# Kernel tuning notes

Measured on AMD Instinct MI355X. Metric: run time of the kernel, lower is better.

## Reference

```python
import jax, jax.numpy as jnp
import numpy as np

B, N, C, H, NRES = 32, 1024, 384, 1024, 20
NTAB = 21  # 20 aa + unknown, per AlphaFold residue_constants


def setup_inputs() -> dict:
    key = jax.random.key(0)
    ks = jax.random.split(key, 16)
    s = 0.02
    inp = {}
    inp['act'] = jax.random.normal(ks[0], (B, N, C), jnp.float32)
    inp['angles'] = jax.random.normal(ks[1], (B, N, 7, 2), jnp.float32)
    inp['rigids'] = jax.random.normal(ks[2], (B, N, 7), jnp.float32)
    inp['fixed_mask'] = jax.random.randint(ks[3], (B, N), 0, 2, jnp.int32)
    inp['seq_t'] = jax.random.randint(ks[4], (B, N), 0, NRES, jnp.int32)
    inp['residx_atom37_to_atom14'] = jax.random.randint(ks[5], (B, N, 37), 0, 14, jnp.int32)
    inp['ln_g'] = jnp.ones((C,), jnp.float32)
    inp['ln_b'] = jnp.zeros((C,), jnp.float32)
    inp['w1'] = jax.random.normal(ks[6], (C, H), jnp.float32) * s
    inp['b1'] = jnp.zeros((H,), jnp.float32)
    inp['w2'] = jax.random.normal(ks[7], (H, H), jnp.float32) * s
    inp['b2'] = jnp.zeros((H,), jnp.float32)
    inp['w3'] = jax.random.normal(ks[8], (H, NRES), jnp.float32) * s
    inp['b3'] = jnp.zeros((NRES,), jnp.float32)
    # stand-in residue_constants tables (same shapes/dtypes as AlphaFold's)
    inp['default_frames'] = jax.random.normal(ks[9], (NTAB, 8, 4, 4), jnp.float32)
    inp['group_idx'] = jax.random.randint(ks[10], (NTAB, 14), 0, 8, jnp.int32)
    inp['atom14_mask'] = (jax.random.uniform(ks[11], (NTAB, 14)) > 0.3).astype(jnp.float32)
    inp['atom37_mask'] = (jax.random.uniform(ks[12], (NTAB, 37)) > 0.3).astype(jnp.float32)
    inp['lit_positions'] = jax.random.normal(ks[13], (NTAB, 14, 3), jnp.float32)
    return inp


def quat_to_rot(q):
    q = q / jnp.sqrt(jnp.sum(q * q, axis=-1, keepdims=True) + 1e-8)
    w, x, y, z = q[..., 0], q[..., 1], q[..., 2], q[..., 3]
    r = jnp.stack([
        1 - 2 * (y * y + z * z), 2 * (x * y - w * z), 2 * (x * z + w * y),
        2 * (x * y + w * z), 1 - 2 * (x * x + z * z), 2 * (y * z - w * x),
        2 * (x * z - w * y), 2 * (y * z + w * x), 1 - 2 * (x * x + y * y)
    ], axis=-1)
    return r.reshape(q.shape[:-1] + (3, 3))


def compose(r1, t1, r2, t2):
    # rigid composition: (r1, t1) o (r2, t2)
    return (jnp.einsum('...ij,...jk->...ik', r1, r2),
            jnp.einsum('...ij,...j->...i', r1, t2) + t1)


def reference(act, angles, rigids, fixed_mask, seq_t, residx_atom37_to_atom14,
              ln_g, ln_b, w1, b1, w2, b2, w3, b3,
              default_frames, group_idx, atom14_mask, atom37_mask, lit_positions):
    # --- small MLP head ---
    mu = jnp.mean(act, axis=-1, keepdims=True)
    var = jnp.var(act, axis=-1, keepdims=True)
    h = (act - mu) / jnp.sqrt(var + 1e-5) * ln_g + ln_b
    h = jax.nn.relu(h @ w1 + b1)
    h = jax.nn.relu(h @ w2 + b2)
    logits = h @ w3 + b3                                # [B,N,20]
    p_0t = jax.nn.softmax(logits, axis=-1)
    seq0 = jnp.argmax(p_0t, axis=-1).astype(jnp.int32)
    seq0 = seq0 * (1 - fixed_mask) + seq_t * fixed_mask  # [B,N]

    # --- backbone frame from quaternion rigids ---
    rb = quat_to_rot(rigids[..., :4])                    # [B,N,3,3]
    tb = rigids[..., 4:]                                 # [B,N,3]

    # --- torsion_angles_to_frames ---
    df = default_frames[seq0]                            # [B,N,8,4,4]
    dr, dt = df[..., :3, :3], df[..., :3, 3]
    sin, cos = angles[..., 0], angles[..., 1]            # [B,N,7]
    z1 = jnp.zeros_like(sin[..., :1])
    sin8 = jnp.concatenate([z1, sin], axis=-1)           # backbone group has angle 0
    cos8 = jnp.concatenate([jnp.ones_like(z1), cos], axis=-1)
    zz, oo = jnp.zeros_like(sin8), jnp.ones_like(sin8)
    rx = jnp.stack([oo, zz, zz, zz, cos8, -sin8, zz, sin8, cos8], axis=-1)
    rx = rx.reshape(sin8.shape + (3, 3))                 # rotation about x-axis
    fr = jnp.einsum('bngij,bngjk->bngik', dr, rx)        # frames to backbone (pre-chain)
    ft = dt
    # chain chi2->chi1, chi3->chi2, chi4->chi3
    r5, t5 = compose(fr[..., 4, :, :], ft[..., 4, :], fr[..., 5, :, :], ft[..., 5, :])
    r6, t6 = compose(r5, t5, fr[..., 6, :, :], ft[..., 6, :])
    r7, t7 = compose(r6, t6, fr[..., 7, :, :], ft[..., 7, :])
    frot = jnp.concatenate([fr[..., :5, :, :], r5[..., None, :, :], r6[..., None, :, :], r7[..., None, :, :]], axis=-3)
    ftr = jnp.concatenate([ft[..., :5, :], t5[..., None, :], t6[..., None, :], t7[..., None, :]], axis=-2)
    grot, gtr = compose(rb[..., None, :, :], tb[..., None, :], frot, ftr)  # [B,N,8,3,3],[B,N,8,3]

    # --- frames_and_literature_positions_to_atom14_pos ---
    gi = group_idx[seq0]                                 # [B,N,14]
    ar = jnp.take_along_axis(grot, jnp.broadcast_to(gi[..., None, None], gi.shape + (3, 3)), axis=2)
    at = jnp.take_along_axis(gtr, jnp.broadcast_to(gi[..., None], gi.shape + (3,)), axis=2)
    lit = lit_positions[seq0]                            # [B,N,14,3]
    m14 = atom14_mask[seq0]                              # [B,N,14]
    pred = (jnp.einsum('bnaij,bnaj->bnai', ar, lit) + at) * m14[..., None]

    # --- atom14 -> atom37 gather ---
    idx = residx_atom37_to_atom14
    final = jnp.take_along_axis(pred, jnp.broadcast_to(idx[..., None], idx.shape + (3,)), axis=2)
    m37 = atom37_mask[seq0]                              # [B,N,37]
    return logits, seq0, pred, final, m14, m37
```

## Files before the change

kernel.cpp:

```cpp
#include <hip/hip_runtime.h>
#include <math.h>

#define B_ 32
#define N_ 1024
#define C_ 384
#define H_ 1024
#define NRES 20
#define NTAB 21
#define M_TOTAL (B_*N_)
#define BK 32

typedef __attribute__((ext_vector_type(8))) short bf16x8;
typedef __attribute__((ext_vector_type(4))) float f32x4;

#define GLOAD_LDS(gptr, lptr) \
    __builtin_amdgcn_global_load_lds( \
        (const __attribute__((address_space(1))) void*)(gptr), \
        (__attribute__((address_space(3))) void*)(lptr), 16, 0, 0)

__device__ inline short bf16_rne(float v) {
    unsigned u = __float_as_uint(v);
    unsigned r = u + 0x7fffu + ((u >> 16) & 1u);
    return (short)(r >> 16);
}
__device__ inline void split2(float v, short& h, short& l) {
    unsigned u = __float_as_uint(v);
    unsigned r = (u + 0x7fffu + ((u >> 16) & 1u)) & 0xffff0000u;
    h = (short)(r >> 16);
    l = bf16_rne(v - __uint_as_float(r));
}

__global__ __launch_bounds__(256) void ln_split_kernel(const float* __restrict__ act,
                                                       const float* __restrict__ lng,
                                                       const float* __restrict__ lnb,
                                                       short* __restrict__ Xh,
                                                       short* __restrict__ Xl) {
    int wave = threadIdx.x >> 6;
    int lane = threadIdx.x & 63;
    int row  = blockIdx.x * 4 + wave;
    const float* x = act + (size_t)row * C_;
    float v[6];
    float s = 0.f;
#pragma unroll
    for (int i = 0; i < 6; i++) { v[i] = x[lane + i*64]; s += v[i]; }
#pragma unroll
    for (int off = 32; off > 0; off >>= 1) s += __shfl_xor(s, off, 64);
    float mu = s * (1.0f/384.0f);
    float vs = 0.f;
#pragma unroll
    for (int i = 0; i < 6; i++) { float d = v[i]-mu; vs += d*d; }
#pragma unroll
    for (int off = 32; off > 0; off >>= 1) vs += __shfl_xor(vs, off, 64);
    float rstd = 1.0f / sqrtf(vs * (1.0f/384.0f) + 1e-5f);
#pragma unroll
    for (int i = 0; i < 6; i++) {
        int col = lane + i*64;
        float y = (v[i] - mu) * rstd * lng[col] + lnb[col];
        short h, l; split2(y, h, l);
        Xh[(size_t)row * C_ + col] = h;
        Xl[(size_t)row * C_ + col] = l;
    }
}

__global__ __launch_bounds__(256) void conv_w_kernel(const float* __restrict__ w,
                                                     short* __restrict__ th,
                                                     short* __restrict__ tl,
                                                     int K, int N, int Npad) {
    __shared__ float t[32][33];
    int n0 = blockIdx.x * 32, k0 = blockIdx.y * 32;
    int tx = threadIdx.x & 31, ty = threadIdx.x >> 5;
#pragma unroll
    for (int i = ty; i < 32; i += 8) {
        int k = k0 + i, n = n0 + tx;
        t[i][tx] = (n < N) ? w[(size_t)k * N + n] : 0.f;
    }
    __syncthreads();
#pragma unroll
    for (int i = ty; i < 32; i += 8) {
        int n = n0 + i, k = k0 + tx;
        short h, l; split2(t[tx][i], h, l);
        th[(size_t)n * K + k] = h;
        tl[(size_t)n * K + k] = l;
    }
}

__global__ __launch_bounds__(512, 2) void presplit_gemm256(
    const short* __restrict__ Ahg, const short* __restrict__ Alg,
    const short* __restrict__ BTh, const short* __restrict__ BTl,
    const float* __restrict__ bias,
    short* __restrict__ Ch, short* __restrict__ Cl,
    int K, int ldc)
{
    __shared__ short P[4][2][256][32];
    const int BUFS = 256*32;
    int tid = threadIdx.x;
    int m0 = blockIdx.x * 256;
    int n0 = blockIdx.y * 256;
    int lane = tid & 63, wv = tid >> 6;
    int wr = wv >> 2, wc = wv & 3;
    int fm = lane & 15, kg = lane >> 4;

    int pl = wv >> 1, hf = wv & 1;
    const short* gsrc = (pl == 0) ? Ahg : (pl == 1) ? Alg : (pl == 2) ? BTh : BTl;
    int base = (pl < 2) ? m0 : n0;
    int swcb = (lane & 3) ^ ((lane >> 3) & 3);
    const short* gp = gsrc + (size_t)(base + hf*128 + (lane >> 2)) * K + swcb * 8;
    short* lpl = &P[pl][0][0][0] + hf * (128*32);

    int sz = (kg ^ ((fm >> 1) & 3)) * 8;
    const short* raH = &P[0][0][wr*128 + fm][0] + sz;
    const short* raL = &P[1][0][wr*128 + fm][0] + sz;
    const short* rbH = &P[2][0][wc*64  + fm][0] + sz;
    const short* rbL = &P[3][0][wc*64  + fm][0] + sz;

#define STAGE(c, bsel, koff) \
    GLOAD_LDS(gp + (size_t)((c)*16) * K + (koff), lpl + (bsel)*BUFS + (c)*512)

#define TRIPLE(ai, aj, AH, AL, BH, BL) { \
    f32x4 cc = acc[ai][aj]; \
    cc = __builtin_amdgcn_mfma_f32_16x16x32_bf16(AL, BH, cc, 0, 0, 0); \
    cc = __builtin_amdgcn_mfma_f32_16x16x32_bf16(AH, BL, cc, 0, 0, 0); \
    cc = __builtin_amdgcn_mfma_f32_16x16x32_bf16(AH, BH, cc, 0, 0, 0); \
    acc[ai][aj] = cc; }

    f32x4 acc[8][4] = {};
    const int NT = K / BK;

#pragma unroll
    for (int c = 0; c < 8; c++) STAGE(c, 0, 0);

    for (int t = 0; t < NT; ++t) {
        int cur = t & 1, nxt = cur ^ 1;
        size_t koff = (size_t)(t + 1) * BK;
        bool pf = (t + 1 < NT);

        bf16x8 a_h[4], a_l[4], b_h[4], b_l[4];

        if (pf) {
            STAGE(0, nxt, koff); STAGE(1, nxt, koff);
            asm volatile("s_waitcnt vmcnt(2)" ::: "memory");
        } else {
            asm volatile("s_waitcnt vmcnt(0)" ::: "memory");
        }
        __builtin_amdgcn_s_barrier();
        __builtin_amdgcn_sched_barrier(0);
#pragma unroll
        for (int i = 0; i < 4; i++) {
            a_h[i] = *(const bf16x8*)(raH + cur*BUFS + i*512);
            a_l[i] = *(const bf16x8*)(raL + cur*BUFS + i*512);
        }
#pragma unroll
        for (int j = 0; j < 2; j++) {
            b_h[j] = *(const bf16x8*)(rbH + cur*BUFS + j*512);
            b_l[j] = *(const bf16x8*)(rbL + cur*BUFS + j*512);
        }
        __builtin_amdgcn_s_setprio(1);
#pragma unroll
        for (int i = 0; i < 4; i++)
#pragma unroll
            for (int j = 0; j < 2; j++) TRIPLE(i, j, a_h[i], a_l[i], b_h[j], b_l[j]);
        __builtin_amdgcn_s_setprio(0);
        __builtin_amdgcn_s_barrier();

        if (pf) { STAGE(2, nxt, koff); STAGE(3, nxt, koff); }
#pragma unroll
        for (int j = 0; j < 2; j++) {
            b_h[2+j] = *(const bf16x8*)(rbH + cur*BUFS + (2+j)*512);
            b_l[2+j] = *(const bf16x8*)(rbL + cur*BUFS + (2+j)*512);
        }
        __builtin_amdgcn_s_barrier();
        __builtin_amdgcn_s_setprio(1);
#pragma unroll
        for (int i = 0; i < 4; i++)
#pragma unroll
            for (int j = 0; j < 2; j++) TRIPLE(i, 2+j, a_h[i], a_l[i], b_h[2+j], b_l[2+j]);
        __builtin_amdgcn_s_setprio(0);
        __builtin_amdgcn_s_barrier();

        if (pf) { STAGE(4, nxt, koff); STAGE(5, nxt, koff); }
#pragma unroll
        for (int i = 0; i < 4; i++) {
            a_h[i] = *(const bf16x8*)(raH + cur*BUFS + (4+i)*512);
            a_l[i] = *(const bf16x8*)(raL + cur*BUFS + (4+i)*512);
        }
        __builtin_amdgcn_s_barrier();
        __builtin_amdgcn_s_setprio(1);
#pragma unroll
        for (int i = 0; i < 4; i++)
#pragma unroll
            for (int j = 0; j < 2; j++) TRIPLE(4+i, j, a_h[i], a_l[i], b_h[j], b_l[j]);
        __builtin_amdgcn_s_setprio(0);
        __builtin_amdgcn_s_barrier();

        if (pf) { STAGE(6, nxt, koff); STAGE(7, nxt, koff); }
        __builtin_amdgcn_s_barrier();
        __builtin_amdgcn_s_setprio(1);
#pragma unroll
        for (int i = 0; i < 4; i++)
#pragma unroll
            for (int j = 0; j < 2; j++) TRIPLE(4+i, 2+j, a_h[i], a_l[i], b_h[2+j], b_l[2+j]);
        __builtin_amdgcn_s_setprio(0);
        __builtin_amdgcn_s_barrier();
    }

#pragma unroll
    for (int i = 0; i < 8; i++)
#pragma unroll
        for (int j = 0; j < 4; j++) {
            int col = n0 + wc*64 + j*16 + fm;
            float bs = bias[col];
#pragma unroll
            for (int r = 0; r < 4; r++) {
                int row = m0 + wr*128 + i*16 + kg*4 + r;
                float v = fmaxf(acc[i][j][r] + bs, 0.f);
                short h, l; split2(v, h, l);
                Ch[(size_t)row * ldc + col] = h;
                Cl[(size_t)row * ldc + col] = l;
            }
        }
#undef STAGE
#undef TRIPLE
}

__global__ __launch_bounds__(256) void gemm3_fused(
    const short* __restrict__ Ahg, const short* __restrict__ Alg,
    const short* __restrict__ BTh, const short* __restrict__ BTl,
    const float* __restrict__ b3,
    const int* __restrict__ fixed_mask, const int* __restrict__ seq_t,
    float* __restrict__ out_logits, float* __restrict__ seq_out,
    int* __restrict__ seq_int, int m0c)
{
    __shared__ short Ah[2][64][32], Al[2][64][32];
    __shared__ short Bh[2][32][32], Bl[2][32][32];
    __shared__ float slog[64][33];
    int tid = threadIdx.x;
    int m0 = blockIdx.x * 64;
    int lane = tid & 63, wv = tid >> 6;
    int wm = wv * 16;
    int fm = lane & 15, kg = lane >> 4;

    const short* gsrc = (wv == 0) ? Ahg : (wv == 1) ? Alg : (wv == 2) ? BTh : BTl;
    short* lb0 = (wv == 0) ? &Ah[0][0][0] : (wv == 1) ? &Al[0][0][0]
               : (wv == 2) ? &Bh[0][0][0] : &Bl[0][0][0];
    int pstride = (wv < 2) ? (64*32) : (32*32);
    int ncalls  = (wv < 2) ? 4 : 2;
    int base = (wv < 2) ? m0 : 0;
    int swcb = (lane & 3) ^ ((lane >> 3) & 3);
    const short* gp = gsrc + (size_t)(base + (lane >> 2)) * H_ + swcb * 8;

    int saz = (kg ^ (((wm + fm) >> 1) & 3)) * 8;
    int sbz[2];
#pragma unroll
    for (int j = 0; j < 2; j++) sbz[j] = (kg ^ (((j*16 + fm) >> 1) & 3)) * 8;

    f32x4 acc[2] = {};
    const int NT = H_ / BK;

    for (int c = 0; c < ncalls; c++)
        GLOAD_LDS(gp + (size_t)(c * 16) * H_, lb0 + c * 512);

    for (int t = 0; t < NT; ++t) {
        __syncthreads();

        if (t + 1 < NT) {
            short* lb = lb0 + ((t + 1) & 1) * pstride;
            size_t k0n = (size_t)(t + 1) * BK;
            for (int c = 0; c < ncalls; c++)
                GLOAD_LDS(gp + (size_t)(c * 16) * H_ + k0n, lb + c * 512);
        }

        int cur = t & 1;
        bf16x8 a_h = *(bf16x8*)&Ah[cur][wm + fm][saz];
        bf16x8 a_l = *(bf16x8*)&Al[cur][wm + fm][saz];
        bf16x8 b_h[2], b_l[2];
#pragma unroll
        for (int j = 0; j < 2; j++) {
            b_h[j] = *(bf16x8*)&Bh[cur][j*16 + fm][sbz[j]];
            b_l[j] = *(bf16x8*)&Bl[cur][j*16 + fm][sbz[j]];
        }
#pragma unroll
        for (int j = 0; j < 2; j++) {
            f32x4 c = acc[j];
            c = __builtin_amdgcn_mfma_f32_16x16x32_bf16(a_l, b_h[j], c, 0, 0, 0);
            c = __builtin_amdgcn_mfma_f32_16x16x32_bf16(a_h, b_l[j], c, 0, 0, 0);
            c = __builtin_amdgcn_mfma_f32_16x16x32_bf16(a_h, b_h[j], c, 0, 0, 0);
            acc[j] = c;
        }
    }

#pragma unroll
    for (int j = 0; j < 2; j++)
#pragma unroll
        for (int r = 0; r < 4; r++)
            slog[wm + kg*4 + r][j*16 + fm] = acc[j][r];
    __syncthreads();

    if (tid < 64) {
        int grow = m0c + m0 + tid;
        float best = -1e30f; int bi = 0;
        float* lg = out_logits + (size_t)grow * NRES;
#pragma unroll
        for (int n = 0; n < NRES; n++) {
            float s = slog[tid][n] + b3[n];
            lg[n] = s;
            if (s > best) { best = s; bi = n; }
        }
        int fmk = fixed_mask[grow];
        int s = fmk ? seq_t[grow] : bi;
        seq_int[grow] = s;
        seq_out[grow] = (float)s;
    }
}

__global__ __launch_bounds__(128) void geom_kernel(
    const float* __restrict__ angles, const float* __restrict__ rigids,
    const int* __restrict__ seq0i, const int* __restrict__ residx,
    const float* __restrict__ dframes, const int* __restrict__ gidx,
    const float* __restrict__ a14m, const float* __restrict__ a37m,
    const float* __restrict__ litp,
    float* __restrict__ out_pred, float* __restrict__ out_final,
    float* __restrict__ out_m14, float* __restrict__ out_m37)
{
    __shared__ float sdf[NTAB*8*16];
    __shared__ int   sgi[NTAB*14];
    __shared__ float sm14[NTAB*14];
    __shared__ float sm37[NTAB*37];
    __shared__ float slit[NTAB*14*3];
    __shared__ float predL[128][43];

    for (int i = threadIdx.x; i < NTAB*128; i += 128) sdf[i] = dframes[i];
    for (int i = threadIdx.x; i < NTAB*14; i += 128) { sgi[i] = gidx[i]; sm14[i] = a14m[i]; }
    for (int i = threadIdx.x; i < NTAB*37; i += 128) sm37[i] = a37m[i];
    for (int i = threadIdx.x; i < NTAB*42; i += 128) slit[i] = litp[i];
    __syncthreads();

    int p = blockIdx.x * 128 + threadIdx.x;
    int s = seq0i[p];

    const float* rg = rigids + (size_t)p * 7;
    float qw = rg[0], qx = rg[1], qy = rg[2], qz = rg[3];
    float tbx = rg[4], tby = rg[5], tbz = rg[6];
    float qn = 1.0f / sqrtf(qw*qw + qx*qx + qy*qy + qz*qz + 1e-8f);
    qw *= qn; qx *= qn; qy *= qn; qz *= qn;
    float rb[9];
    rb[0] = 1.f - 2.f*(qy*qy + qz*qz); rb[1] = 2.f*(qx*qy - qw*qz); rb[2] = 2.f*(qx*qz + qw*qy);
    rb[3] = 2.f*(qx*qy + qw*qz); rb[4] = 1.f - 2.f*(qx*qx + qz*qz); rb[5] = 2.f*(qy*qz - qw*qx);
    rb[6] = 2.f*(qx*qz - qw*qy); rb[7] = 2.f*(qy*qz + qw*qx); rb[8] = 1.f - 2.f*(qx*qx + qy*qy);

    float fr[8][9], ft[8][3];
    const float* ang = angles + (size_t)p * 14;
#pragma unroll
    for (int g = 0; g < 8; g++) {
        const float* df = &sdf[(s*8 + g)*16];
        float c, sn;
        if (g == 0) { c = 1.f; sn = 0.f; }
        else { sn = ang[(g-1)*2 + 0]; c = ang[(g-1)*2 + 1]; }
#pragma unroll
        for (int i = 0; i < 3; i++) {
            float d0 = df[i*4+0], d1 = df[i*4+1], d2 = df[i*4+2];
            fr[g][i*3+0] = d0;
            fr[g][i*3+1] = d1*c + d2*sn;
            fr[g][i*3+2] = d2*c - d1*sn;
            ft[g][i] = df[i*4+3];
        }
    }
#pragma unroll
    for (int g = 5; g <= 7; g++) {
        float r[9], t[3];
        const float* r1 = fr[g-1];
        const float* t1 = ft[g-1];
#pragma unroll
        for (int i = 0; i < 3; i++) {
#pragma unroll
            for (int j = 0; j < 3; j++)
                r[i*3+j] = r1[i*3+0]*fr[g][0*3+j] + r1[i*3+1]*fr[g][1*3+j] + r1[i*3+2]*fr[g][2*3+j];
            t[i] = r1[i*3+0]*ft[g][0] + r1[i*3+1]*ft[g][1] + r1[i*3+2]*ft[g][2] + t1[i];
        }
#pragma unroll
        for (int i = 0; i < 9; i++) fr[g][i] = r[i];
#pragma unroll
        for (int i = 0; i < 3; i++) ft[g][i] = t[i];
    }
#pragma unroll
    for (int g = 0; g < 8; g++) {
        float r[9], t[3];
#pragma unroll
        for (int i = 0; i < 3; i++) {
#pragma unroll
            for (int j = 0; j < 3; j++)
                r[i*3+j] = rb[i*3+0]*fr[g][0*3+j] + rb[i*3+1]*fr[g][1*3+j] + rb[i*3+2]*fr[g][2*3+j];
            t[i] = rb[i*3+0]*ft[g][0] + rb[i*3+1]*ft[g][1] + rb[i*3+2]*ft[g][2];
        }
#pragma unroll
        for (int i = 0; i < 9; i++) fr[g][i] = r[i];
        ft[g][0]=t[0]+tbx; ft[g][1]=t[1]+tby; ft[g][2]=t[2]+tbz;
    }
#pragma unroll
    for (int g = 0; g < 8; g++) {
#pragma unroll
        for (int a = 0; a < 14; a++) {
            if (sgi[s*14 + a] == g) {
                float m  = sm14[s*14 + a];
                float lx = slit[(s*14 + a)*3 + 0];
                float ly = slit[(s*14 + a)*3 + 1];
                float lz = slit[(s*14 + a)*3 + 2];
                float px = (fr[g][0]*lx + fr[g][1]*ly + fr[g][2]*lz + ft[g][0]) * m;
                float py = (fr[g][3]*lx + fr[g][4]*ly + fr[g][5]*lz + ft[g][1]) * m;
                float pz = (fr[g][6]*lx + fr[g][7]*ly + fr[g][8]*lz + ft[g][2]) * m;
                predL[threadIdx.x][a*3+0] = px;
                predL[threadIdx.x][a*3+1] = py;
                predL[threadIdx.x][a*3+2] = pz;
                out_pred[((size_t)p*14 + a)*3 + 0] = px;
                out_pred[((size_t)p*14 + a)*3 + 1] = py;
                out_pred[((size_t)p*14 + a)*3 + 2] = pz;
            }
        }
    }
#pragma unroll
    for (int a = 0; a < 14; a++) out_m14[(size_t)p*14 + a] = sm14[s*14 + a];

    const int* idx = residx + (size_t)p * 37;
#pragma unroll
    for (int a = 0; a < 37; a++) {
        int id = idx[a];
        out_final[((size_t)p*37 + a)*3 + 0] = predL[threadIdx.x][id*3+0];
        out_final[((size_t)p*37 + a)*3 + 1] = predL[threadIdx.x][id*3+1];
        out_final[((size_t)p*37 + a)*3 + 2] = predL[threadIdx.x][id*3+2];
        out_m37[(size_t)p*37 + a] = sm37[s*37 + a];
    }
}

extern "C" void kernel_launch(void* const* d_in, const int* in_sizes, int n_in,
                              void* d_out, int out_size, void* d_ws, size_t ws_size,
                              hipStream_t stream) {
    const float* act        = (const float*)d_in[0];
    const float* angles     = (const float*)d_in[1];
    const float* rigids     = (const float*)d_in[2];
    const int*   fixed_mask = (const int*)d_in[3];
    const int*   seq_t      = (const int*)d_in[4];
    const int*   residx     = (const int*)d_in[5];
    const float* lng        = (const float*)d_in[6];
    const float* lnb        = (const float*)d_in[7];
    const float* w1         = (const float*)d_in[8];
    const float* b1         = (const float*)d_in[9];
    const float* w2         = (const float*)d_in[10];
    const float* b2         = (const float*)d_in[11];
    const float* w3         = (const float*)d_in[12];
    const float* b3         = (const float*)d_in[13];
    const float* dfr        = (const float*)d_in[14];
    const int*   gidx       = (const int*)d_in[15];
    const float* a14m       = (const float*)d_in[16];
    const float* a37m       = (const float*)d_in[17];
    const float* litp       = (const float*)d_in[18];

    float* out        = (float*)d_out;
    float* out_logits = out;
    float* out_seq    = out_logits + (size_t)M_TOTAL * NRES;
    float* out_pred   = out_seq    + (size_t)M_TOTAL;
    float* out_final  = out_pred   + (size_t)M_TOTAL * 42;
    float* out_m14    = out_final  + (size_t)M_TOTAL * 111;
    float* out_m37    = out_m14    + (size_t)M_TOTAL * 14;

    char* wsp = (char*)d_ws;
    int*   seq0i = (int*)wsp;   wsp += (size_t)M_TOTAL * sizeof(int);
    short* w1h   = (short*)wsp; wsp += (size_t)H_ * C_ * sizeof(short);
    short* w1l   = (short*)wsp; wsp += (size_t)H_ * C_ * sizeof(short);
    short* w2h   = (short*)wsp; wsp += (size_t)H_ * H_ * sizeof(short);
    short* w2l   = (short*)wsp; wsp += (size_t)H_ * H_ * sizeof(short);
    short* w3h   = (short*)wsp; wsp += (size_t)128 * H_ * sizeof(short);
    short* w3l   = (short*)wsp; wsp += (size_t)128 * H_ * sizeof(short);
    short* Xh    = (short*)wsp; wsp += (size_t)M_TOTAL * C_ * sizeof(short);
    short* Xl    = (short*)wsp; wsp += (size_t)M_TOTAL * C_ * sizeof(short);

    size_t fixed_bytes = (size_t)(wsp - (char*)d_ws);
    size_t per_row = 4ull * H_ * sizeof(short);
    size_t avail = ws_size - fixed_bytes;
    int chunkM = 4096;
    if (avail >= (size_t)M_TOTAL * per_row)      chunkM = M_TOTAL;
    else if (avail >= 16384ull * per_row)        chunkM = 16384;
    else if (avail >= 8192ull * per_row)         chunkM = 8192;

    short* H1h = (short*)wsp; wsp += (size_t)chunkM * H_ * sizeof(short);
    short* H1l = (short*)wsp; wsp += (size_t)chunkM * H_ * sizeof(short);
    short* H2h = (short*)wsp; wsp += (size_t)chunkM * H_ * sizeof(short);
    short* H2l = (short*)wsp;

    conv_w_kernel<<<dim3(H_/32, C_/32), 256, 0, stream>>>(w1, w1h, w1l, C_, H_, H_);
    conv_w_kernel<<<dim3(H_/32, H_/32), 256, 0, stream>>>(w2, w2h, w2l, H_, H_, H_);
    conv_w_kernel<<<dim3(128/32, H_/32), 256, 0, stream>>>(w3, w3h, w3l, H_, NRES, 128);

    ln_split_kernel<<<M_TOTAL/4, 256, 0, stream>>>(act, lng, lnb, Xh, Xl);

    for (int c = 0; c < M_TOTAL / chunkM; c++) {
        int m0 = c * chunkM;
        presplit_gemm256<<<dim3(chunkM/256, H_/256), 512, 0, stream>>>(
            Xh + (size_t)m0 * C_, Xl + (size_t)m0 * C_, w1h, w1l, b1, H1h, H1l, C_, H_);
        presplit_gemm256<<<dim3(chunkM/256, H_/256), 512, 0, stream>>>(
            H1h, H1l, w2h, w2l, b2, H2h, H2l, H_, H_);
        gemm3_fused<<<chunkM/64, 256, 0, stream>>>(H2h, H2l, w3h, w3l, b3,
                                                   fixed_mask, seq_t,
                                                   out_logits, out_seq, seq0i, m0);
    }

    geom_kernel<<<M_TOTAL/128, 128, 0, stream>>>(angles, rigids, seq0i, residx,
                                                 dfr, gidx, a14m, a37m, litp,
                                                 out_pred, out_final, out_m14, out_m37);
}
```

Measured before the change: 462.9 us.

## Restructure GEMM main loop to issue all prefetches up front and preload next A fragments

The bf16x3 GEMM main loop is reorganised so all eight global-to-LDS prefetch loads for the next K tile are issued at once at the start of each iteration, not interleaved across four phases. Separate register sets for the two A and B halves let the MFMA quadrants be reordered so the next tile's first A fragments are read from LDS before the last quadrant. This removes some barriers and the partial vmcnt waits, aiming to overlap LDS reads with MFMA work. In exchange it uses more VGPRs, which may lower occupancy, and issues memory traffic in a burst.

```diff
diff --git a/kernel.cpp b/kernel.cpp
--- a/kernel.cpp
+++ b/kernel.cpp
@@ -113,8 +113,10 @@
     const short* rbH = &P[2][0][wc*64  + fm][0] + sz;
     const short* rbL = &P[3][0][wc*64  + fm][0] + sz;
 
-#define STAGE(c, bsel, koff) \
-    GLOAD_LDS(gp + (size_t)((c)*16) * K + (koff), lpl + (bsel)*BUFS + (c)*512)
+#define STAGE8(bsel, koff) \
+    { _Pragma("unroll") \
+      for (int c = 0; c < 8; c++) \
+          GLOAD_LDS(gp + (size_t)(c*16) * K + (koff), lpl + (bsel)*BUFS + c*512); }
 
 #define TRIPLE(ai, aj, AH, AL, BH, BL) { \
     f32x4 cc = acc[ai][aj]; \
@@ -126,79 +128,73 @@
     f32x4 acc[8][4] = {};
     const int NT = K / BK;
 
-#pragma unroll
-    for (int c = 0; c < 8; c++) STAGE(c, 0, 0);
+    bf16x8 aAh[4], aAl[4], aBh[4], aBl[4];
+    bf16x8 bAh[2], bAl[2], bBh[2], bBl[2];
+
+    STAGE8(0, 0);
+    asm volatile("s_waitcnt vmcnt(0)" ::: "memory");
+    __builtin_amdgcn_s_barrier();
+#pragma unroll
+    for (int i = 0; i < 4; i++) {
+        aAh[i] = *(const bf16x8*)(raH + i*512);
+        aAl[i] = *(const bf16x8*)(raL + i*512);
+    }
 
     for (int t = 0; t < NT; ++t) {
         int cur = t & 1, nxt = cur ^ 1;
         size_t koff = (size_t)(t + 1) * BK;
         bool pf = (t + 1 < NT);
 
-        bf16x8 a_h[4], a_l[4], b_h[4], b_l[4];
-
-        if (pf) {
-            STAGE(0, nxt, koff); STAGE(1, nxt, koff);
-            asm volatile("s_waitcnt vmcnt(2)" ::: "memory");
-        } else {
-            asm volatile("s_waitcnt vmcnt(0)" ::: "memory");
-        }
-        __builtin_amdgcn_s_barrier();
-        __builtin_amdgcn_sched_barrier(0);
-#pragma unroll
-        for (int i = 0; i < 4; i++) {
-            a_h[i] = *(const bf16x8*)(raH + cur*BUFS + i*512);
-            a_l[i] = *(const bf16x8*)(raL + cur*BUFS + i*512);
-        }
 #pragma unroll
         for (int j = 0; j < 2; j++) {
-            b_h[j] = *(const bf16x8*)(rbH + cur*BUFS + j*512);
-            b_l[j] = *(const bf16x8*)(rbL + cur*BUFS + j*512);
-        }
+            bAh[j] = *(const bf16x8*)(rbH + cur*BUFS + j*512);
+            bAl[j] = *(const bf16x8*)(rbL + cur*BUFS + j*512);
+            bBh[j] = *(const bf16x8*)(rbH + cur*BUFS + (2+j)*512);
+            bBl[j] = *(const bf16x8*)(rbL + cur*BUFS + (2+j)*512);
+        }
+        if (pf) STAGE8(nxt, koff);
         __builtin_amdgcn_s_setprio(1);
 #pragma unroll
         for (int i = 0; i < 4; i++)
 #pragma unroll
-            for (int j = 0; j < 2; j++) TRIPLE(i, j, a_h[i], a_l[i], b_h[j], b_l[j]);
+            for (int j = 0; j < 2; j++) TRIPLE(i, j, aAh[i], aAl[i], bAh[j], bAl[j]);
         __builtin_amdgcn_s_setprio(0);
         __builtin_amdgcn_s_barrier();
 
-        if (pf) { STAGE(2, nxt, koff); STAGE(3, nxt, koff); }
-#pragma unroll
-        for (int j = 0; j < 2; j++) {
-            b_h[2+j] = *(const bf16x8*)(rbH + cur*BUFS + (2+j)*512);
-            b_l[2+j] = *(const bf16x8*)(rbL + cur*BUFS + (2+j)*512);
-        }
-        __builtin_amdgcn_s_barrier();
+#pragma unroll
+        for (int i = 0; i < 4; i++) {
+            aBh[i] = *(const bf16x8*)(raH + cur*BUFS + (4+i)*512);
+            aBl[i] = *(const bf16x8*)(raL + cur*BUFS + (4+i)*512);
+        }
         __builtin_amdgcn_s_setprio(1);
 #pragma unroll
         for (int i = 0; i < 4; i++)
 #pragma unroll
-            for (int j = 0; j < 2; j++) TRIPLE(i, 2+j, a_h[i], a_l[i], b_h[2+j], b_l[2+j]);
+            for (int j = 0; j < 2; j++) TRIPLE(i, 2+j, aAh[i], aAl[i], bBh[j], bBl[j]);
         __builtin_amdgcn_s_setprio(0);
         __builtin_amdgcn_s_barrier();
 
-        if (pf) { STAGE(4, nxt, koff); STAGE(5, nxt, koff); }
-#pragma unroll
-        for (int i = 0; i < 4; i++) {
-            a_h[i] = *(const bf16x8*)(raH + cur*BUFS + (4+i)*512);
-            a_l[i] = *(const bf16x8*)(raL + cur*BUFS + (4+i)*512);
-        }
+        __builtin_amdgcn_s_setprio(1);
+#pragma unroll
+        for (int i = 0; i < 4; i++)
+#pragma unroll
+            for (int j = 0; j < 2; j++) TRIPLE(4+i, 2+j, aBh[i], aBl[i], bBh[j], bBl[j]);
+        __builtin_amdgcn_s_setprio(0);
+        asm volatile("s_waitcnt vmcnt(0)" ::: "memory");
         __builtin_amdgcn_s_barrier();
+
+        if (pf) {
+#pragma unroll
+            for (int i = 0; i < 4; i++) {
+                aAh[i] = *(const bf16x8*)(raH + nxt*BUFS + i*512);
+                aAl[i] = *(const bf16x8*)(raL + nxt*BUFS + i*512);
+            }
+        }
         __builtin_amdgcn_s_setprio(1);
 #pragma unroll
         for (int i = 0; i < 4; i++)
 #pragma unroll
-            for (int j = 0; j < 2; j++) TRIPLE(4+i, j, a_h[i], a_l[i], b_h[j], b_l[j]);
-        __builtin_amdgcn_s_setprio(0);
-        __builtin_amdgcn_s_barrier();
-
-        if (pf) { STAGE(6, nxt, koff); STAGE(7, nxt, koff); }
-        __builtin_amdgcn_s_barrier();
-        __builtin_amdgcn_s_setprio(1);
-#pragma unroll
-        for (int i = 0; i < 4; i++)
-#pragma unroll
-            for (int j = 0; j < 2; j++) TRIPLE(4+i, 2+j, a_h[i], a_l[i], b_h[2+j], b_l[2+j]);
+            for (int j = 0; j < 2; j++) TRIPLE(4+i, j, aBh[i], aBl[i], bAh[j], bAl[j]);
         __builtin_amdgcn_s_setprio(0);
         __builtin_amdgcn_s_barrier();
     }
@@ -218,7 +214,7 @@
                 Cl[(size_t)row * ldc + col] = l;
             }
         }
-#undef STAGE
+#undef STAGE8
 #undef TRIPLE
 }
 
```

Measured after the change: 475.5 us. +2.7%, slower.

## Fuse third GEMM into second GEMM epilogue with atomic logit accumulation

Applied to the files above, without the earlier changes.

The second MLP GEMM no longer writes its hidden activation to global memory. Instead each 256x256 tile stores the ReLU'd split-bf16 result in LDS and multiplies it immediately by the matching K-slice of w3, accumulating partial logits into the output with atomicAdd. A separate small kernel then adds the bias and does the argmax. This removes the write and re-read of the large H2 buffer and the standalone third GEMM, at the cost of atomics across four column blocks per row, a memset, and an epilogue that reads w3 directly from global memory.

```diff
diff --git a/kernel.cpp b/kernel.cpp
--- a/kernel.cpp
+++ b/kernel.cpp
@@ -84,12 +84,15 @@
     }
 }
 
+template<bool FUSE>
 __global__ __launch_bounds__(512, 2) void presplit_gemm256(
     const short* __restrict__ Ahg, const short* __restrict__ Alg,
     const short* __restrict__ BTh, const short* __restrict__ BTl,
     const float* __restrict__ bias,
     short* __restrict__ Ch, short* __restrict__ Cl,
-    int K, int ldc)
+    int K, int ldc,
+    const short* __restrict__ W3h, const short* __restrict__ W3l,
+    float* __restrict__ logit_acc, int m0c)
 {
     __shared__ short P[4][2][256][32];
     const int BUFS = 256*32;
@@ -203,113 +206,103 @@
         __builtin_amdgcn_s_barrier();
     }
 
-#pragma unroll
-    for (int i = 0; i < 8; i++)
-#pragma unroll
-        for (int j = 0; j < 4; j++) {
-            int col = n0 + wc*64 + j*16 + fm;
-            float bs = bias[col];
-#pragma unroll
-            for (int r = 0; r < 4; r++) {
-                int row = m0 + wr*128 + i*16 + kg*4 + r;
-                float v = fmaxf(acc[i][j][r] + bs, 0.f);
-                short h, l; split2(v, h, l);
-                Ch[(size_t)row * ldc + col] = h;
-                Cl[(size_t)row * ldc + col] = l;
+    if (!FUSE) {
+#pragma unroll
+        for (int i = 0; i < 8; i++)
+#pragma unroll
+            for (int j = 0; j < 4; j++) {
+                int col = n0 + wc*64 + j*16 + fm;
+                float bs = bias[col];
+#pragma unroll
+                for (int r2 = 0; r2 < 4; r2++) {
+                    int row = m0 + wr*128 + i*16 + kg*4 + r2;
+                    float v = fmaxf(acc[i][j][r2] + bs, 0.f);
+                    short h, l; split2(v, h, l);
+                    Ch[(size_t)row * ldc + col] = h;
+                    Cl[(size_t)row * ldc + col] = l;
+                }
             }
-        }
+    } else {
+        unsigned* L32 = (unsigned*)&P[0][0][0][0];
+#pragma unroll
+        for (int h = 0; h < 2; h++) {
+            if (wr == h) {
+#pragma unroll
+                for (int i = 0; i < 8; i++)
+#pragma unroll
+                    for (int j = 0; j < 4; j++) {
+                        int col = wc*64 + j*16 + fm;
+                        float bs = bias[n0 + col];
+#pragma unroll
+                        for (int r2 = 0; r2 < 4; r2++) {
+                            int lr = i*16 + kg*4 + r2;
+                            float v = fmaxf(acc[i][j][r2] + bs, 0.f);
+                            short sh, sl; split2(v, sh, sl);
+                            L32[lr*256 + (col ^ ((lr & 15) << 1))] =
+                                ((unsigned)(unsigned short)sh << 16) | (unsigned short)sl;
+                        }
+                    }
+            }
+            __syncthreads();
+            f32x4 pl0 = {}, pl1 = {};
+            int rbase = (wv*16 + fm) * 256;
+            int swr = fm << 1;
+#pragma unroll
+            for (int s = 0; s < 8; s++) {
+                int kb = s*32 + kg*8;
+                bf16x8 A_h, A_l;
+#pragma unroll
+                for (int c = 0; c < 8; c++) {
+                    unsigned u = L32[rbase + ((kb + c) ^ swr)];
+                    A_h[c] = (short)(u >> 16);
+                    A_l[c] = (short)(u & 0xffffu);
+                }
+                size_t wk = (size_t)(n0 + kb);
+                bf16x8 B0h = *(const bf16x8*)&W3h[(size_t)fm * H_ + wk];
+                bf16x8 B0l = *(const bf16x8*)&W3l[(size_t)fm * H_ + wk];
+                bf16x8 B1h = *(const bf16x8*)&W3h[(size_t)(16 + fm) * H_ + wk];
+                bf16x8 B1l = *(const bf16x8*)&W3l[(size_t)(16 + fm) * H_ + wk];
+                pl0 = __builtin_amdgcn_mfma_f32_16x16x32_bf16(A_l, B0h, pl0, 0, 0, 0);
+                pl0 = __builtin_amdgcn_mfma_f32_16x16x32_bf16(A_h, B0l, pl0, 0, 0, 0);
+                pl0 = __builtin_amdgcn_mfma_f32_16x16x32_bf16(A_h, B0h, pl0, 0, 0, 0);
+                pl1 = __builtin_amdgcn_mfma_f32_16x16x32_bf16(A_l, B1h, pl1, 0, 0, 0);
+                pl1 = __builtin_amdgcn_mfma_f32_16x16x32_bf16(A_h, B1l, pl1, 0, 0, 0);
+                pl1 = __builtin_amdgcn_mfma_f32_16x16x32_bf16(A_h, B1h, pl1, 0, 0, 0);
+            }
+            int growb = m0c + m0 + h*128 + wv*16 + kg*4;
+#pragma unroll
+            for (int r2 = 0; r2 < 4; r2++)
+                atomicAdd(&logit_acc[(size_t)(growb + r2) * NRES + fm], pl0[r2]);
+            if (fm < 4) {
+#pragma unroll
+                for (int r2 = 0; r2 < 4; r2++)
+                    atomicAdd(&logit_acc[(size_t)(growb + r2) * NRES + 16 + fm], pl1[r2]);
+            }
+            __syncthreads();
+        }
+    }
 #undef STAGE
 #undef TRIPLE
 }
 
-__global__ __launch_bounds__(256) void gemm3_fused(
-    const short* __restrict__ Ahg, const short* __restrict__ Alg,
-    const short* __restrict__ BTh, const short* __restrict__ BTl,
-    const float* __restrict__ b3,
+__global__ __launch_bounds__(256) void argmax_kernel(
+    float* __restrict__ logits, const float* __restrict__ b3,
     const int* __restrict__ fixed_mask, const int* __restrict__ seq_t,
-    float* __restrict__ out_logits, float* __restrict__ seq_out,
-    int* __restrict__ seq_int, int m0c)
+    float* __restrict__ seq_out, int* __restrict__ seq_int, int m0c)
 {
-    __shared__ short Ah[2][64][32], Al[2][64][32];
-    __shared__ short Bh[2][32][32], Bl[2][32][32];
-    __shared__ float slog[64][33];
-    int tid = threadIdx.x;
-    int m0 = blockIdx.x * 64;
-    int lane = tid & 63, wv = tid >> 6;
-    int wm = wv * 16;
-    int fm = lane & 15, kg = lane >> 4;
-
-    const short* gsrc = (wv == 0) ? Ahg : (wv == 1) ? Alg : (wv == 2) ? BTh : BTl;
-    short* lb0 = (wv == 0) ? &Ah[0][0][0] : (wv == 1) ? &Al[0][0][0]
-               : (wv == 2) ? &Bh[0][0][0] : &Bl[0][0][0];
-    int pstride = (wv < 2) ? (64*32) : (32*32);
-    int ncalls  = (wv < 2) ? 4 : 2;
-    int base = (wv < 2) ? m0 : 0;
-    int swcb = (lane & 3) ^ ((lane >> 3) & 3);
-    const short* gp = gsrc + (size_t)(base + (lane >> 2)) * H_ + swcb * 8;
-
-    int saz = (kg ^ (((wm + fm) >> 1) & 3)) * 8;
-    int sbz[2];
-#pragma unroll
-    for (int j = 0; j < 2; j++) sbz[j] = (kg ^ (((j*16 + fm) >> 1) & 3)) * 8;
-
-    f32x4 acc[2] = {};
-    const int NT = H_ / BK;
-
-    for (int c = 0; c < ncalls; c++)
-        GLOAD_LDS(gp + (size_t)(c * 16) * H_, lb0 + c * 512);
-
-    for (int t = 0; t < NT; ++t) {
-        __syncthreads();
-
-        if (t + 1 < NT) {
-            short* lb = lb0 + ((t + 1) & 1) * pstride;
-            size_t k0n = (size_t)(t + 1) * BK;
-            for (int c = 0; c < ncalls; c++)
-                GLOAD_LDS(gp + (size_t)(c * 16) * H_ + k0n, lb + c * 512);
-        }
-
-        int cur = t & 1;
-        bf16x8 a_h = *(bf16x8*)&Ah[cur][wm + fm][saz];
-        bf16x8 a_l = *(bf16x8*)&Al[cur][wm + fm][saz];
-        bf16x8 b_h[2], b_l[2];
-#pragma unroll
-        for (int j = 0; j < 2; j++) {
-            b_h[j] = *(bf16x8*)&Bh[cur][j*16 + fm][sbz[j]];
-            b_l[j] = *(bf16x8*)&Bl[cur][j*16 + fm][sbz[j]];
-        }
-#pragma unroll
-        for (int j = 0; j < 2; j++) {
-            f32x4 c = acc[j];
-            c = __builtin_amdgcn_mfma_f32_16x16x32_bf16(a_l, b_h[j], c, 0, 0, 0);
-            c = __builtin_amdgcn_mfma_f32_16x16x32_bf16(a_h, b_l[j], c, 0, 0, 0);
-            c = __builtin_amdgcn_mfma_f32_16x16x32_bf16(a_h, b_h[j], c, 0, 0, 0);
-            acc[j] = c;
-        }
-    }
-
-#pragma unroll
-    for (int j = 0; j < 2; j++)
-#pragma unroll
-        for (int r = 0; r < 4; r++)
-            slog[wm + kg*4 + r][j*16 + fm] = acc[j][r];
-    __syncthreads();
-
-    if (tid < 64) {
-        int grow = m0c + m0 + tid;
-        float best = -1e30f; int bi = 0;
-        float* lg = out_logits + (size_t)grow * NRES;
-#pragma unroll
-        for (int n = 0; n < NRES; n++) {
-            float s = slog[tid][n] + b3[n];
-            lg[n] = s;
-            if (s > best) { best = s; bi = n; }
-        }
-        int fmk = fixed_mask[grow];
-        int s = fmk ? seq_t[grow] : bi;
-        seq_int[grow] = s;
-        seq_out[grow] = (float)s;
-    }
+    int grow = m0c + blockIdx.x * 256 + threadIdx.x;
+    float* lg = logits + (size_t)grow * NRES;
+    float best = -1e30f; int bi = 0;
+#pragma unroll
+    for (int n = 0; n < NRES; n++) {
+        float s = lg[n] + b3[n];
+        lg[n] = s;
+        if (s > best) { best = s; bi = n; }
+    }
+    int fmk = fixed_mask[grow];
+    int sv = fmk ? seq_t[grow] : bi;
+    seq_int[grow] = sv;
+    seq_out[grow] = (float)sv;
 }
 
 __global__ __launch_bounds__(128) void geom_kernel(
@@ -473,7 +466,7 @@
     short* Xl    = (short*)wsp; wsp += (size_t)M_TOTAL * C_ * sizeof(short);
 
     size_t fixed_bytes = (size_t)(wsp - (char*)d_ws);
-    size_t per_row = 4ull * H_ * sizeof(short);
+    size_t per_row = 2ull * H_ * sizeof(short);
     size_t avail = ws_size - fixed_bytes;
     int chunkM = 4096;
     if (avail >= (size_t)M_TOTAL * per_row)      chunkM = M_TOTAL;
@@ -481,9 +474,9 @@
     else if (avail >= 8192ull * per_row)         chunkM = 8192;
 
     short* H1h = (short*)wsp; wsp += (size_t)chunkM * H_ * sizeof(short);
-    short* H1l = (short*)wsp; wsp += (size_t)chunkM * H_ * sizeof(short);
-    short* H2h = (short*)wsp; wsp += (size_t)chunkM * H_ * sizeof(short);
-    short* H2l = (short*)wsp;
+    short* H1l = (short*)wsp;
+
+    hipMemsetAsync(out_logits, 0, (size_t)M_TOTAL * NRES * sizeof(float), stream);
 
     conv_w_kernel<<<dim3(H_/32, C_/32), 256, 0, stream>>>(w1, w1h, w1l, C_, H_, H_);
     conv_w_kernel<<<dim3(H_/32, H_/32), 256, 0, stream>>>(w2, w2h, w2l, H_, H_, H_);
@@ -493,13 +486,14 @@
 
     for (int c = 0; c < M_TOTAL / chunkM; c++) {
         int m0 = c * chunkM;
-        presplit_gemm256<<<dim3(chunkM/256, H_/256), 512, 0, stream>>>(
-            Xh + (size_t)m0 * C_, Xl + (size_t)m0 * C_, w1h, w1l, b1, H1h, H1l, C_, H_);
-        presplit_gemm256<<<dim3(chunkM/256, H_/256), 512, 0, stream>>>(
-            H1h, H1l, w2h, w2l, b2, H2h, H2l, H_, H_);
-        gemm3_fused<<<chunkM/64, 256, 0, stream>>>(H2h, H2l, w3h, w3l, b3,
-                                                   fixed_mask, seq_t,
-                                                   out_logits, out_seq, seq0i, m0);
+        presplit_gemm256<false><<<dim3(chunkM/256, H_/256), 512, 0, stream>>>(
+            Xh + (size_t)m0 * C_, Xl + (size_t)m0 * C_, w1h, w1l, b1,
+            H1h, H1l, C_, H_, nullptr, nullptr, nullptr, 0);
+        presplit_gemm256<true><<<dim3(chunkM/256, H_/256), 512, 0, stream>>>(
+            H1h, H1l, w2h, w2l, b2,
+            nullptr, nullptr, H_, 0, w3h, w3l, out_logits, m0);
+        argmax_kernel<<<chunkM/256, 256, 0, stream>>>(
+            out_logits, b3, fixed_mask, seq_t, out_seq, seq0i, m0);
     }
 
     geom_kernel<<<M_TOTAL/128, 128, 0, stream>>>(angles, rigids, seq0i, residx,
```

After: 467.9 us. About the same (+1.1%).
